# Kernel tuning notes

Hardware: AMD Instinct MI355X
Metric: run time of the kernel (lower is better)

## Reference

```python
import jax, jax.numpy as jnp
import numpy as np

B, T, D = 64, 8192, 128

def setup_inputs() -> dict:
    key = jax.random.key(0)
    ks = jax.random.split(key, 6)
    H_r = jax.random.normal(ks[0], (B, T, D), dtype=jnp.float32)
    mask_r = jax.random.randint(ks[1], (B, T), 0, 2, dtype=jnp.int32)
    h_tm1 = jax.random.normal(ks[2], (B, D), dtype=jnp.float32)
    # xavier-ish scaling for linear weights
    s = 1.0 / np.sqrt(D)
    V_w = jax.random.normal(ks[3], (D, D), dtype=jnp.float32) * s
    Wa_w = jax.random.normal(ks[4], (D, D), dtype=jnp.float32) * s
    V_b = jnp.zeros((D,), dtype=jnp.float32)
    Wa_b = jnp.zeros((D,), dtype=jnp.float32)
    v = jax.random.normal(ks[5], (D,), dtype=jnp.float32) * 0.05
    c = jnp.ones((1,), dtype=jnp.float32)
    return {"H_r": H_r, "mask_r": mask_r, "h_tm1": h_tm1, "V_w": V_w,
            "V_b": V_b, "Wa_w": Wa_w, "Wa_b": Wa_b, "v": v, "c": c}

def masked_softmax(x, m, axis=-1):
    x = jnp.clip(x, -15.0, 15.0)
    x = x * m
    e_x = jnp.exp(x - jnp.max(x, axis=axis, keepdims=True))
    e_x = e_x * m
    return e_x / (jnp.sum(e_x, axis=axis, keepdims=True) + 1e-6)

def reference(H_r, mask_r, h_tm1, V_w, V_b, Wa_w, Wa_b, v, c):
    m = mask_r.astype(jnp.float32)                      # [B,T]
    Fk = jnp.einsum('btd,od->bto', H_r, V_w) + V_b      # [B,T,D]
    Fk_prime = h_tm1 @ Wa_w.T + Wa_b                    # [B,D]
    Fk = jnp.tanh(Fk + Fk_prime[:, None, :])
    beta = Fk @ v + c                                   # [B,T]
    beta = masked_softmax(beta, m, axis=-1)
    z = jnp.einsum('bt,btd->bd', beta, H_r)             # [B,D]
    return (z, beta)
```

## Files before the change

### kernel.cpp

```cpp
#include <hip/hip_runtime.h>
#include <math.h>

#define BB 64
#define TT 8192
#define DD 128
#define RPT 64
#define NT 8
#define RPBLK (RPT * NT)
#define NBLK (BB * TT / RPBLK)
#define BPB (TT / RPBLK)

typedef float f32x4 __attribute__((ext_vector_type(4)));
typedef __bf16 bf16x4 __attribute__((ext_vector_type(4)));
typedef __bf16 bf16x8 __attribute__((ext_vector_type(8)));

__device__ __forceinline__ float fast_tanh(float x) {
    float t = __expf(2.f * x);
    return 1.f - 2.f * __builtin_amdgcn_rcpf(t + 1.f);
}

__device__ __forceinline__ float bf_at_lo16(unsigned u) { return __uint_as_float(u << 16); }
__device__ __forceinline__ float bf_at_hi16(unsigned u) { return __uint_as_float(u & 0xffff0000u); }

__global__ __launch_bounds__(256) void convw_kernel(const float* __restrict__ Vw,
                                                    __bf16* __restrict__ Vw_bf) {
    const int i = blockIdx.x * 256 + threadIdx.x;
    const int r = i >> 7, cidx = i & 127;
    Vw_bf[r * DD + (cidx ^ ((r & 7) << 3))] = (__bf16)Vw[i];
}

__global__ __launch_bounds__(DD) void fkprime_kernel(
    const float* __restrict__ Waw, const float* __restrict__ Wab,
    const float* __restrict__ h_tm1, float* __restrict__ fkp) {
    const int b = blockIdx.x;
    const int o = threadIdx.x;
    const float* __restrict__ w = Waw + o * DD;
    const float* __restrict__ h = h_tm1 + b * DD;
    float a0 = 0.f, a1 = 0.f, a2 = 0.f, a3 = 0.f;
#pragma unroll
    for (int d = 0; d < DD; d += 4) {
        float4 w4 = *reinterpret_cast<const float4*>(w + d);
        a0 = fmaf(w4.x, h[d + 0], a0);
        a1 = fmaf(w4.y, h[d + 1], a1);
        a2 = fmaf(w4.z, h[d + 2], a2);
        a3 = fmaf(w4.w, h[d + 3], a3);
    }
    fkp[b * DD + o] = (a0 + a1) + (a2 + a3) + Wab[o];
}

__global__ __launch_bounds__(256, 2) void beta_z_kernel(
    const float* __restrict__ H, const __bf16* __restrict__ Vw_bf,
    const float* __restrict__ Vb, const float* __restrict__ fkp,
    const float* __restrict__ vvec, const float* __restrict__ cptr,
    const int* __restrict__ mask,
    float* __restrict__ eout,
    float* __restrict__ zpart) {
    const int tid  = threadIdx.x;
    const int wv   = tid >> 6;
    const int lane = tid & 63;
    const int cl   = lane & 15;
    const int kg   = lane >> 4;
    const int base_row = blockIdx.x * RPBLK;
    const int b    = base_row >> 13;

    __shared__ short s_vw[DD * DD];
    __shared__ short s_h[2][RPT * DD];
    __shared__ float s_ep[RPT];
    __shared__ float s_z[4][DD];

    {
        const char* __restrict__ wg = (const char*)Vw_bf;
#pragma unroll
        for (int i = 0; i < 8; ++i) {
            __builtin_amdgcn_global_load_lds(
                (const void*)(wg + i * 4096 + wv * 1024 + lane * 16),
                (void*)((char*)s_vw + i * 4096 + wv * 1024), 16, 0, 0);
        }
    }
    float4 hreg[8];
    {
        const float4* __restrict__ Hg =
            reinterpret_cast<const float4*>(H + (size_t)base_row * DD);
#pragma unroll
        for (int i = 0; i < 8; ++i) hreg[i] = Hg[i * 256 + tid];
#pragma unroll
        for (int i = 0; i < 8; ++i) {
            bf16x4 r;
            r[0] = (__bf16)hreg[i].x; r[1] = (__bf16)hreg[i].y;
            r[2] = (__bf16)hreg[i].z; r[3] = (__bf16)hreg[i].w;
            const int off  = (i * 256 + tid) * 8;
            const int trow = off >> 8;
            *reinterpret_cast<bf16x4*>((char*)s_h[0] + (off ^ ((trow & 7) << 4))) = r;
        }
    }
    __syncthreads();

    const float cval = cptr[0];
    const int   ra   = wv * 16 + cl;
    const int   swzA = (ra & 7) << 4;
    const int   dp   = tid & 63;
    const int   tg   = tid >> 6;
    float za0 = 0.f, za1 = 0.f;

    for (int t = 0; t < NT; ++t) {
        const int cur = t & 1;

        if (t + 1 < NT) {
            const float4* __restrict__ Hn = reinterpret_cast<const float4*>(
                H + (size_t)(base_row + (t + 1) * RPT) * DD);
#pragma unroll
            for (int i = 0; i < 8; ++i) hreg[i] = Hn[i * 256 + tid];
        }

        f32x4 acc[8];
#pragma unroll
        for (int nt = 0; nt < 8; ++nt) acc[nt] = (f32x4){0.f, 0.f, 0.f, 0.f};
#pragma unroll
        for (int kk = 0; kk < 4; ++kk) {
            const int abyte = ra * 256 + kk * 64 + kg * 16;
            bf16x8 af = *reinterpret_cast<const bf16x8*>(
                (char*)s_h[cur] + (abyte ^ swzA));
#pragma unroll
            for (int nt = 0; nt < 8; ++nt) {
                const int rb    = nt * 16 + cl;
                const int bbyte = (rb * 256 + kk * 64 + kg * 16) ^ ((rb & 7) << 4);
                bf16x8 bfr = *reinterpret_cast<const bf16x8*>((const char*)s_vw + bbyte);
                acc[nt] = __builtin_amdgcn_mfma_f32_16x16x32_bf16(af, bfr, acc[nt], 0, 0, 0);
            }
        }

        float part[4] = {0.f, 0.f, 0.f, 0.f};
#pragma unroll
        for (int nt = 0; nt < 8; ++nt) {
            const int col = nt * 16 + cl;
            const float bias = Vb[col] + fkp[b * DD + col];
            const float vvl  = vvec[col];
#pragma unroll
            for (int j = 0; j < 4; ++j)
                part[j] = fmaf(fast_tanh(acc[nt][j] + bias), vvl, part[j]);
        }
#pragma unroll
        for (int off = 1; off < 16; off <<= 1) {
#pragma unroll
            for (int j = 0; j < 4; ++j) part[j] += __shfl_xor(part[j], off);
        }
        if (cl == 0) {
#pragma unroll
            for (int j = 0; j < 4; ++j) {
                const int lrow = wv * 16 + kg * 4 + j;
                const int g    = base_row + t * RPT + lrow;
                float x  = fminf(fmaxf(cval + part[j], -15.f), 15.f);
                float mv = (float)mask[g];
                float ep = __expf(x * mv - 15.f) * mv;
                eout[g] = ep;
                s_ep[lrow] = ep;
            }
        }
        __syncthreads();

        for (int tt = tg; tt < RPT; tt += 4) {
            const unsigned hv = *reinterpret_cast<const unsigned*>(
                (char*)s_h[cur] + ((tt * 256 + dp * 4) ^ ((tt & 7) << 4)));
            const float w = s_ep[tt];
            za0 = fmaf(w, bf_at_lo16(hv), za0);
            za1 = fmaf(w, bf_at_hi16(hv), za1);
        }

        if (t + 1 < NT) {
#pragma unroll
            for (int i = 0; i < 8; ++i) {
                bf16x4 r;
                r[0] = (__bf16)hreg[i].x; r[1] = (__bf16)hreg[i].y;
                r[2] = (__bf16)hreg[i].z; r[3] = (__bf16)hreg[i].w;
                const int off  = (i * 256 + tid) * 8;
                const int trow = off >> 8;
                *reinterpret_cast<bf16x4*>(
                    (char*)s_h[cur ^ 1] + (off ^ ((trow & 7) << 4))) = r;
            }
        }
        __syncthreads();
    }

    s_z[tg][dp * 2]     = za0;
    s_z[tg][dp * 2 + 1] = za1;
    __syncthreads();
    if (tid < DD) {
        zpart[(size_t)blockIdx.x * DD + tid] =
            (s_z[0][tid] + s_z[1][tid]) + (s_z[2][tid] + s_z[3][tid]);
    }
}

__global__ __launch_bounds__(256) void denom_kernel(
    float* __restrict__ eout, const int* __restrict__ mask,
    float* __restrict__ denom) {
    const int b = blockIdx.x, tid = threadIdx.x;
    float* __restrict__ e = eout + (size_t)b * TT;
    const int* __restrict__ mrow = mask + (size_t)b * TT;
    __shared__ float sE[256], sM[256];
    __shared__ int sA[256];

    float E = 0.f, M = 0.f;
    int any0 = 0;
    for (int t = tid; t < TT; t += 256) {
        float ep = e[t];
        E += ep;
        M = fmaxf(M, ep);
        any0 |= (mrow[t] == 0);
    }
    sE[tid] = E; sM[tid] = M; sA[tid] = any0;
    __syncthreads();
    for (int s = 128; s > 0; s >>= 1) {
        if (tid < s) {
            sE[tid] += sE[tid + s];
            sM[tid] = fmaxf(sM[tid], sM[tid + s]);
            sA[tid] |= sA[tid + s];
        }
        __syncthreads();
    }
    const float scale = sA[0] ? fmaxf(sM[0], 3.0590232e-7f ) : sM[0];
    const float dn = sE[0] + 1e-6f * scale;
    if (tid == 0) denom[b] = dn;
    const float inv = 1.f / dn;
    for (int t = tid; t < TT; t += 256) e[t] *= inv;
}

__global__ __launch_bounds__(256) void zfinal_kernel(
    const float* __restrict__ zpart, const float* __restrict__ denom,
    float* __restrict__ out_z) {
    const int idx = blockIdx.x * 256 + threadIdx.x;
    const int b = idx >> 7, d = idx & 127;
    const float* __restrict__ zp = zpart + (size_t)b * BPB * DD + d;
    float s = 0.f;
#pragma unroll
    for (int cc = 0; cc < BPB; ++cc) s += zp[cc * DD];
    out_z[idx] = s / denom[b];
}

extern "C" void kernel_launch(void* const* d_in, const int* in_sizes, int n_in,
                              void* d_out, int out_size, void* d_ws, size_t ws_size,
                              hipStream_t stream) {
    const float* H     = (const float*)d_in[0];
    const int*   mask  = (const int*)d_in[1];
    const float* h_tm1 = (const float*)d_in[2];
    const float* V_w   = (const float*)d_in[3];
    const float* V_b   = (const float*)d_in[4];
    const float* Wa_w  = (const float*)d_in[5];
    const float* Wa_b  = (const float*)d_in[6];
    const float* v     = (const float*)d_in[7];
    const float* c     = (const float*)d_in[8];

    float* out_z    = (float*)d_out;
    float* out_beta = (float*)d_out + BB * DD;

    float* ws     = (float*)d_ws;
    float* fkp    = ws;
    float* zpart  = fkp + BB * DD;
    float* denom  = zpart + NBLK * DD;
    __bf16* Vw_bf = (__bf16*)(denom + BB);

    convw_kernel<<<(DD * DD) / 256, 256, 0, stream>>>(V_w, Vw_bf);
    fkprime_kernel<<<BB, DD, 0, stream>>>(Wa_w, Wa_b, h_tm1, fkp);
    beta_z_kernel<<<NBLK, 256, 0, stream>>>(H, Vw_bf, V_b, fkp, v, c, mask,
                                            out_beta, zpart);
    denom_kernel<<<BB, 256, 0, stream>>>(out_beta, mask, denom);
    zfinal_kernel<<<(BB * DD) / 256, 256, 0, stream>>>(zpart, denom, out_z);
}
```

Before: 94.70 us.

## Make each wave own its H rows to drop block barriers and double buffer

Each wave now loads, converts and consumes only its own 16 rows of H per tile. The z accumulation reads softmax weights via cross-lane shuffles instead of shared memory, which removes both per-iteration __syncthreads and the second H buffer in LDS. The smaller LDS footprint allows raising the launch bound to 3 blocks per CU, and the bias and v values are hoisted out of the loop. The risks are higher register pressure under the tighter bound and a possible hazard, since a wave overwrites its own LDS rows with no intra-wave barrier.

```diff
diff --git a/kernel.cpp b/kernel.cpp
--- a/kernel.cpp
+++ b/kernel.cpp
@@ -48,7 +48,7 @@
     fkp[b * DD + o] = (a0 + a1) + (a2 + a3) + Wab[o];
 }
 
-__global__ __launch_bounds__(256, 2) void beta_z_kernel(
+__global__ __launch_bounds__(256, 3) void beta_z_kernel(
     const float* __restrict__ H, const __bf16* __restrict__ Vw_bf,
     const float* __restrict__ Vb, const float* __restrict__ fkp,
     const float* __restrict__ vvec, const float* __restrict__ cptr,
@@ -64,8 +64,7 @@
     const int b    = base_row >> 13;
 
     __shared__ short s_vw[DD * DD];
-    __shared__ short s_h[2][RPT * DD];
-    __shared__ float s_ep[RPT];
+    __shared__ short s_h[RPT * DD];
     __shared__ float s_z[4][DD];
 
     {
@@ -79,47 +78,53 @@
     }
     float4 hreg[8];
     {
-        const float4* __restrict__ Hg =
-            reinterpret_cast<const float4*>(H + (size_t)base_row * DD);
-#pragma unroll
-        for (int i = 0; i < 8; ++i) hreg[i] = Hg[i * 256 + tid];
+        const float4* __restrict__ H4 =
+            reinterpret_cast<const float4*>(H + (size_t)(base_row + wv * 16) * DD);
+#pragma unroll
+        for (int i = 0; i < 8; ++i) hreg[i] = H4[i * 64 + lane];
 #pragma unroll
         for (int i = 0; i < 8; ++i) {
             bf16x4 r;
             r[0] = (__bf16)hreg[i].x; r[1] = (__bf16)hreg[i].y;
             r[2] = (__bf16)hreg[i].z; r[3] = (__bf16)hreg[i].w;
-            const int off  = (i * 256 + tid) * 8;
-            const int trow = off >> 8;
-            *reinterpret_cast<bf16x4*>((char*)s_h[0] + (off ^ ((trow & 7) << 4))) = r;
+            const int off = wv * 4096 + (i * 64 + lane) * 8;
+            const int row = off >> 8;
+            *reinterpret_cast<bf16x4*>((char*)s_h + (off ^ ((row & 7) << 4))) = r;
         }
     }
     __syncthreads();
 
     const float cval = cptr[0];
-    const int   ra   = wv * 16 + cl;
-    const int   swzA = (ra & 7) << 4;
-    const int   dp   = tid & 63;
-    const int   tg   = tid >> 6;
+    float biasv[8], vvv[8];
+#pragma unroll
+    for (int nt = 0; nt < 8; ++nt) {
+        const int col = nt * 16 + cl;
+        biasv[nt] = Vb[col] + fkp[b * DD + col];
+        vvv[nt]   = vvec[col];
+    }
+
+    const int swzA = (cl & 7) << 4;
     float za0 = 0.f, za1 = 0.f;
 
     for (int t = 0; t < NT; ++t) {
-        const int cur = t & 1;
+        const int grow0 = base_row + t * RPT + wv * 16;
 
         if (t + 1 < NT) {
             const float4* __restrict__ Hn = reinterpret_cast<const float4*>(
-                H + (size_t)(base_row + (t + 1) * RPT) * DD);
-#pragma unroll
-            for (int i = 0; i < 8; ++i) hreg[i] = Hn[i * 256 + tid];
-        }
+                H + (size_t)(grow0 + RPT) * DD);
+#pragma unroll
+            for (int i = 0; i < 8; ++i) hreg[i] = Hn[i * 64 + lane];
+        }
+        const float mfl = (float)mask[grow0 + cl];
+        __builtin_amdgcn_sched_barrier(0);
 
         f32x4 acc[8];
 #pragma unroll
         for (int nt = 0; nt < 8; ++nt) acc[nt] = (f32x4){0.f, 0.f, 0.f, 0.f};
 #pragma unroll
         for (int kk = 0; kk < 4; ++kk) {
-            const int abyte = ra * 256 + kk * 64 + kg * 16;
-            bf16x8 af = *reinterpret_cast<const bf16x8*>(
-                (char*)s_h[cur] + (abyte ^ swzA));
+            const int abyte = (wv * 16 + cl) * 256 + kk * 64 + kg * 16;
+            bf16x8 af = *reinterpret_cast<const bf16x8*>((char*)s_h + (abyte ^ swzA));
 #pragma unroll
             for (int nt = 0; nt < 8; ++nt) {
                 const int rb    = nt * 16 + cl;
@@ -132,38 +137,34 @@
         float part[4] = {0.f, 0.f, 0.f, 0.f};
 #pragma unroll
         for (int nt = 0; nt < 8; ++nt) {
-            const int col = nt * 16 + cl;
-            const float bias = Vb[col] + fkp[b * DD + col];
-            const float vvl  = vvec[col];
 #pragma unroll
             for (int j = 0; j < 4; ++j)
-                part[j] = fmaf(fast_tanh(acc[nt][j] + bias), vvl, part[j]);
+                part[j] = fmaf(fast_tanh(acc[nt][j] + biasv[nt]), vvv[nt], part[j]);
         }
 #pragma unroll
         for (int off = 1; off < 16; off <<= 1) {
 #pragma unroll
             for (int j = 0; j < 4; ++j) part[j] += __shfl_xor(part[j], off);
         }
+        float epj[4];
+#pragma unroll
+        for (int j = 0; j < 4; ++j) {
+            const float mv = __shfl(mfl, kg * 4 + j);
+            const float x  = fminf(fmaxf(cval + part[j], -15.f), 15.f);
+            epj[j] = __expf(x * mv - 15.f) * mv;
+        }
         if (cl == 0) {
 #pragma unroll
-            for (int j = 0; j < 4; ++j) {
-                const int lrow = wv * 16 + kg * 4 + j;
-                const int g    = base_row + t * RPT + lrow;
-                float x  = fminf(fmaxf(cval + part[j], -15.f), 15.f);
-                float mv = (float)mask[g];
-                float ep = __expf(x * mv - 15.f) * mv;
-                eout[g] = ep;
-                s_ep[lrow] = ep;
-            }
-        }
-        __syncthreads();
-
-        for (int tt = tg; tt < RPT; tt += 4) {
+            for (int j = 0; j < 4; ++j) eout[grow0 + kg * 4 + j] = epj[j];
+        }
+
+#pragma unroll
+        for (int r = 0; r < 16; ++r) {
+            const float epr = __shfl(epj[r & 3], (r >> 2) << 4);
             const unsigned hv = *reinterpret_cast<const unsigned*>(
-                (char*)s_h[cur] + ((tt * 256 + dp * 4) ^ ((tt & 7) << 4)));
-            const float w = s_ep[tt];
-            za0 = fmaf(w, bf_at_lo16(hv), za0);
-            za1 = fmaf(w, bf_at_hi16(hv), za1);
+                (char*)s_h + (((wv * 16 + r) * 256 + lane * 4) ^ ((r & 7) << 4)));
+            za0 = fmaf(epr, bf_at_lo16(hv), za0);
+            za1 = fmaf(epr, bf_at_hi16(hv), za1);
         }
 
         if (t + 1 < NT) {
@@ -172,17 +173,15 @@
                 bf16x4 r;
                 r[0] = (__bf16)hreg[i].x; r[1] = (__bf16)hreg[i].y;
                 r[2] = (__bf16)hreg[i].z; r[3] = (__bf16)hreg[i].w;
-                const int off  = (i * 256 + tid) * 8;
-                const int trow = off >> 8;
-                *reinterpret_cast<bf16x4*>(
-                    (char*)s_h[cur ^ 1] + (off ^ ((trow & 7) << 4))) = r;
+                const int off = wv * 4096 + (i * 64 + lane) * 8;
+                const int row = off >> 8;
+                *reinterpret_cast<bf16x4*>((char*)s_h + (off ^ ((row & 7) << 4))) = r;
             }
         }
-        __syncthreads();
-    }
-
-    s_z[tg][dp * 2]     = za0;
-    s_z[tg][dp * 2 + 1] = za1;
+    }
+
+    s_z[wv][2 * lane]     = za0;
+    s_z[wv][2 * lane + 1] = za1;
     __syncthreads();
     if (tid < DD) {
         zpart[(size_t)blockIdx.x * DD + tid] =
```

After: 108.1 us. +14.1%, slower.
